# Optimization experiments

Hardware: AMD Instinct MI355X
Metric: run time of the kernel (lower is better)

The kernel has to match this reference:

```python
import jax, jax.numpy as jnp
import numpy as np

EPS = 1e-5


def setup_inputs() -> dict:
    key = jax.random.key(0)
    S, B, I, H, D = 256, 512, 64, 128, 32
    ks = jax.random.split(key, 12)

    def w(k, shape, fan):
        return jax.random.normal(k, shape, jnp.float32) * (fan ** -0.5)

    lengths = jax.random.randint(ks[0], (B,), 1, S + 1)
    lengths = lengths.at[0].set(S)  # ensure max length == S
    return {
        'x': jax.random.normal(ks[1], (S, B, I), jnp.float32),
        'x_d': jax.random.normal(ks[2], (S, B, D), jnp.float32),
        'lengths': lengths,
        'bn_g': jnp.ones((I,), jnp.float32), 'bn_b': jnp.zeros((I,), jnp.float32),
        'bnd_g': jnp.ones((D,), jnp.float32), 'bnd_b': jnp.zeros((D,), jnp.float32),
        'Wih': w(ks[3], (3 * H, I), I), 'Whh': w(ks[4], (3 * H, H), H),
        'bih': jnp.zeros((3 * H,), jnp.float32), 'bhh': jnp.zeros((3 * H,), jnp.float32),
        'attn_W': w(ks[5], (H, H), H), 'attn_b': jnp.zeros((H,), jnp.float32),
        'W1': w(ks[6], (H, H + D), H + D), 'b1': jnp.zeros((H,), jnp.float32),
        'W2': w(ks[7], (H, H), H), 'b2': jnp.zeros((H,), jnp.float32),
        'W3': w(ks[8], (H, H), H), 'b3': jnp.zeros((H,), jnp.float32),
    }


def reference(x, x_d, lengths, bn_g, bn_b, bnd_g, bnd_b, Wih, Whh, bih, bhh,
              attn_W, attn_b, W1, b1, W2, b2, W3, b3):
    S, B, I = x.shape
    H = Whh.shape[1]
    mask = jnp.arange(S)[:, None] < lengths[None, :]          # [S,B] valid-token mask
    mf = mask[..., None].astype(x.dtype)                       # [S,B,1]
    cnt = mf.sum()

    def bn(v, g, b):  # training-mode BatchNorm1d over the packed (valid) tokens
        mu = (v * mf).sum((0, 1)) / cnt
        var = (((v - mu) * mf) ** 2).sum((0, 1)) / cnt
        return (v - mu) * jax.lax.rsqrt(var + EPS) * g + b

    xn = bn(x, bn_g, bn_b)
    xdn = bn(x_d, bnd_g, bnd_b)

    # --- GRU (PyTorch gate order r,z,n) over padded sequence with mask ---
    h0 = jnp.zeros((B, H), x.dtype)

    def step(h, inp):
        xt, mt = inp                                           # xt [B,I], mt [B,1]
        gi = xt @ Wih.T + bih
        gh = h @ Whh.T + bhh
        ir, iz, inn = jnp.split(gi, 3, axis=-1)
        hr, hz, hn = jnp.split(gh, 3, axis=-1)
        r = jax.nn.sigmoid(ir + hr)
        z = jax.nn.sigmoid(iz + hz)
        n = jnp.tanh(inn + r * hn)
        hnew = (1 - z) * n + z * h
        hnext = jnp.where(mt, hnew, h)                         # carry last valid state
        return hnext, jnp.where(mt, hnew, 0.0)                 # padded outputs are 0

    h_last, ys = jax.lax.scan(step, h0, (xn, mf))              # ys [S,B,H]

    # --- Dynamic_Attention: per step i only position j=i survives the causal
    # mask in column k=i, so the dim-0 softmax is over one element -> weight 1.
    # Keep fc in the graph (zero grad, same as torch) via a size-1 softmax. ---
    s = (ys @ attn_W.T + attn_b).sum(-1)                       # [S,B]
    attn = jax.nn.softmax(s[..., None, None], axis=-2)[..., 0, :]  # ones [S,B,1]
    y = attn * ys

    # --- per-token MLP (dropout = identity at eval), vectorized over all tokens ---
    z0 = jnp.concatenate([y, xdn], axis=-1)                    # [S,B,H+D]
    d = jax.nn.relu(z0 @ W1.T + b1)
    d = jax.nn.relu(d @ W2.T + b2)
    d = jax.nn.relu(d @ W3.T + b3)
    out = d * mf                                               # zero padded positions
    return out, h_last[None]                                   # hidden: [1,B,H]
```

## Files before the change

kernel.cpp:

```cpp
#include <hip/hip_runtime.h>
#include <hip/hip_bf16.h>

#define SS 256
#define BB 512
#define II 64
#define HH 128
#define DD 32

typedef __attribute__((ext_vector_type(8))) short short8;
typedef __attribute__((ext_vector_type(4))) float f32x4;

__device__ __forceinline__ short f2bf(float f) {
    unsigned u = __builtin_bit_cast(unsigned, f);
    u += 0x7FFFu + ((u >> 16) & 1u);
    return (short)(u >> 16);
}
__device__ __forceinline__ int pack2bf(float a, float b) {
    return (int)((((unsigned)(unsigned short)f2bf(b)) << 16) |
                  ((unsigned)(unsigned short)f2bf(a)));
}
__device__ __forceinline__ short8 load8bf(const float* p) {
    short8 r;
#pragma unroll
    for (int j = 0; j < 8; ++j) r[j] = f2bf(p[j]);
    return r;
}

__device__ __forceinline__ void sync_lds() {
    __builtin_amdgcn_s_waitcnt(0xc07f);
    __builtin_amdgcn_s_barrier();
}

__global__ __launch_bounds__(256) void stats_kernel(
    const float* __restrict__ x, const float* __restrict__ xd,
    const int* __restrict__ lengths, double* __restrict__ acc,
    unsigned* __restrict__ counter,
    const float* __restrict__ bn_g, const float* __restrict__ bn_b,
    const float* __restrict__ bnd_g, const float* __restrict__ bnd_b,
    float* __restrict__ der)
{
    __shared__ float red_s[256];
    __shared__ float red_q[256];
    __shared__ unsigned s_last;
    const int rows = SS * BB;
    int blk = blockIdx.x;
    const float* v;
    int C, rpb, base;
    if (blk < 256) { v = x;  C = II; rpb = rows / 256; base = 0; }
    else           { v = xd; C = DD; rpb = rows / 128; base = 128; blk -= 256; }

    const int tid = threadIdx.x;
    const int c   = tid & (C - 1);
    const int rg  = tid / C;
    const int rpg = 256 / C;
    const int r0  = blk * rpb;
    const int r1  = r0 + rpb;
    float s = 0.f, q = 0.f;
    for (int r = r0 + rg; r < r1; r += rpg) {
        const int b  = r & (BB - 1);
        const int si = r >> 9;
        if (si < lengths[b]) {
            const float xv = v[(size_t)r * C + c];
            s += xv;
            q  = fmaf(xv, xv, q);
        }
    }
    red_s[tid] = s; red_q[tid] = q;
    __syncthreads();
    if (rg == 0) {
        for (int g = 1; g < rpg; ++g) { s += red_s[c + g * C]; q += red_q[c + g * C]; }
        atomicAdd(&acc[base + c],     (double)s);
        atomicAdd(&acc[base + C + c], (double)q);
    }
    __threadfence();
    __syncthreads();
    if (tid == 0) {
        unsigned old = atomicAdd(counter, 1u);
        s_last = (old == 383u) ? 1u : 0u;
    }
    __syncthreads();
    if (!s_last) return;

    __shared__ int redc[256];
    int cs = 0;
    for (int i = tid; i < BB; i += 256) cs += lengths[i];
    redc[tid] = cs;
    __syncthreads();
    for (int off = 128; off; off >>= 1) {
        if (tid < off) redc[tid] += redc[tid + off];
        __syncthreads();
    }
    const double inv = 1.0 / (double)redc[0];
    if (tid < 64) {
        const double su = __hip_atomic_load(&acc[tid],      __ATOMIC_RELAXED, __HIP_MEMORY_SCOPE_AGENT);
        const double sq = __hip_atomic_load(&acc[64 + tid], __ATOMIC_RELAXED, __HIP_MEMORY_SCOPE_AGENT);
        const double mu  = su * inv;
        const double var = sq * inv - mu * mu;
        const float  rs  = rsqrtf((float)(var + 1e-5));
        const float  a   = rs * bn_g[tid];
        der[tid]      = a;
        der[64 + tid] = bn_b[tid] - (float)mu * a;
    } else if (tid < 96) {
        const int i = tid - 64;
        const double su = __hip_atomic_load(&acc[128 + i], __ATOMIC_RELAXED, __HIP_MEMORY_SCOPE_AGENT);
        const double sq = __hip_atomic_load(&acc[160 + i], __ATOMIC_RELAXED, __HIP_MEMORY_SCOPE_AGENT);
        const double mu  = su * inv;
        const double var = sq * inv - mu * mu;
        const float  rs  = rsqrtf((float)(var + 1e-5));
        const float  a   = rs * bnd_g[i];
        der[128 + i] = a;
        der[160 + i] = bnd_b[i] - (float)mu * a;
    }
}

__global__ __launch_bounds__(512, 2) void gru_kernel(
    const float* __restrict__ x, const int* __restrict__ lengths,
    const float* __restrict__ Wih, const float* __restrict__ Whh,
    const float* __restrict__ bih, const float* __restrict__ bhh,
    const float* __restrict__ der,
    float* __restrict__ ys, float* __restrict__ hlast)
{
    __shared__ __align__(16) short hbf[2][16 * 136];
    __shared__ __align__(16) short xbf[2][16 * 72];

    const int tid  = threadIdx.x;
    const int w    = tid >> 6;
    const int l    = tid & 63;
    const int col  = l & 15;
    const int quad = l >> 4;
    const int b0   = blockIdx.x * 16;
    const int ur   = 16 * w + col;
    const int g0   = 16 * w + quad * 4;

    short8 WR[6], WZ[6], WNh[4], WNx[2];
#pragma unroll
    for (int ks = 0; ks < 4; ++ks) {
        const int ko = ks * 32 + quad * 8;
        WR[ks]  = load8bf(&Whh[(size_t)ur * HH + ko]);
        WZ[ks]  = load8bf(&Whh[(size_t)(HH + ur) * HH + ko]);
        WNh[ks] = load8bf(&Whh[(size_t)(2 * HH + ur) * HH + ko]);
    }
#pragma unroll
    for (int ks = 0; ks < 2; ++ks) {
        const int ko = ks * 32 + quad * 8;
        WR[4 + ks] = load8bf(&Wih[(size_t)ur * II + ko]);
        WZ[4 + ks] = load8bf(&Wih[(size_t)(HH + ur) * II + ko]);
        WNx[ks]    = load8bf(&Wih[(size_t)(2 * HH + ur) * II + ko]);
    }
    float br_[4], bz_[4], bnh_[4], bnx_[4];
#pragma unroll
    for (int r = 0; r < 4; ++r) {
        const int g = g0 + r;
        br_[r]  = bih[g] + bhh[g];
        bz_[r]  = bih[HH + g] + bhh[HH + g];
        bnh_[r] = bhh[2 * HH + g];
        bnx_[r] = bih[2 * HH + g];
    }
    const int len = lengths[b0 + col];

    const int srow = tid >> 5, scol = (tid & 31) * 2;
    const float ax0 = der[scol],      ax1 = der[scol + 1];
    const float cx0 = der[64 + scol], cx1 = der[64 + scol + 1];

    for (int i = tid; i < 16 * 136 / 2; i += 512) ((int*)hbf[0])[i] = 0;
    float hreg[4] = {0.f, 0.f, 0.f, 0.f};
    {
        const float2 xv = *(const float2*)&x[(size_t)(b0 + srow) * II + scol];
        *(int*)&xbf[0][srow * 72 + scol] =
            pack2bf(fmaf(xv.x, ax0, cx0), fmaf(xv.y, ax1, cx1));
    }
    sync_lds();

    int p = 0;
    for (int t = 0; t < SS; ++t) {
        float2 xv;
        if (t + 1 < SS)
            xv = *(const float2*)&x[(size_t)((t + 1) * BB + b0 + srow) * II + scol];

        short8 Hf[4];
#pragma unroll
        for (int ks = 0; ks < 4; ++ks)
            Hf[ks] = *(const short8*)&hbf[p][col * 136 + ks * 32 + quad * 8];
        const short8 XN0 = *(const short8*)&xbf[p][col * 72 + quad * 8];
        const short8 XN1 = *(const short8*)&xbf[p][col * 72 + 32 + quad * 8];

        f32x4 ar  = {br_[0],  br_[1],  br_[2],  br_[3]};
        f32x4 az  = {bz_[0],  bz_[1],  bz_[2],  bz_[3]};
        f32x4 anh = {bnh_[0], bnh_[1], bnh_[2], bnh_[3]};
        f32x4 anx = {bnx_[0], bnx_[1], bnx_[2], bnx_[3]};
#pragma unroll
        for (int ks = 0; ks < 4; ++ks) {
            ar  = __builtin_amdgcn_mfma_f32_16x16x32_bf16(WR[ks],  Hf[ks], ar,  0, 0, 0);
            az  = __builtin_amdgcn_mfma_f32_16x16x32_bf16(WZ[ks],  Hf[ks], az,  0, 0, 0);
            anh = __builtin_amdgcn_mfma_f32_16x16x32_bf16(WNh[ks], Hf[ks], anh, 0, 0, 0);
        }
        ar  = __builtin_amdgcn_mfma_f32_16x16x32_bf16(WR[4],  XN0, ar,  0, 0, 0);
        ar  = __builtin_amdgcn_mfma_f32_16x16x32_bf16(WR[5],  XN1, ar,  0, 0, 0);
        az  = __builtin_amdgcn_mfma_f32_16x16x32_bf16(WZ[4],  XN0, az,  0, 0, 0);
        az  = __builtin_amdgcn_mfma_f32_16x16x32_bf16(WZ[5],  XN1, az,  0, 0, 0);
        anx = __builtin_amdgcn_mfma_f32_16x16x32_bf16(WNx[0], XN0, anx, 0, 0, 0);
        anx = __builtin_amdgcn_mfma_f32_16x16x32_bf16(WNx[1], XN1, anx, 0, 0, 0);

        const bool valid = (t < len);
#pragma unroll
        for (int r = 0; r < 4; ++r) {
            const float rg = __builtin_amdgcn_rcpf(1.f + __expf(-ar[r]));
            const float zg = __builtin_amdgcn_rcpf(1.f + __expf(-az[r]));
            const float nv = anx[r] + rg * anh[r];
            const float ng = 1.f - 2.f * __builtin_amdgcn_rcpf(1.f + __expf(2.f * nv));
            const float hnew = (1.f - zg) * ng + zg * hreg[r];
            hreg[r] = valid ? hnew : hreg[r];
        }
        {
            float4 o;
            o.x = hreg[0]; o.y = hreg[1]; o.z = hreg[2]; o.w = hreg[3];
            *(float4*)&ys[((size_t)t * BB + b0 + col) * HH + g0] = o;
            int2 pk;
            pk.x = pack2bf(hreg[0], hreg[1]);
            pk.y = pack2bf(hreg[2], hreg[3]);
            *(int2*)&hbf[p ^ 1][col * 136 + g0] = pk;
        }
        if (t + 1 < SS)
            *(int*)&xbf[p ^ 1][srow * 72 + scol] =
                pack2bf(fmaf(xv.x, ax0, cx0), fmaf(xv.y, ax1, cx1));

        sync_lds();
        p ^= 1;
    }

    {
        float4 hl;
        hl.x = hreg[0]; hl.y = hreg[1]; hl.z = hreg[2]; hl.w = hreg[3];
        *(float4*)&hlast[(size_t)(b0 + col) * HH + g0] = hl;
    }
}

__global__ __launch_bounds__(512, 2) void mlp_kernel(
    const float* __restrict__ xd, const int* __restrict__ lengths,
    const float* __restrict__ W1, const float* __restrict__ b1v,
    const float* __restrict__ W2, const float* __restrict__ b2v,
    const float* __restrict__ W3, const float* __restrict__ b3v,
    const float* __restrict__ der, float* io)
{
    __shared__ __align__(16) short z0[2][16 * 168];
    __shared__ __align__(16) short d1b[2][16 * 136];
    __shared__ __align__(16) short d2b[2][16 * 136];

    const int tid  = threadIdx.x;
    const int w    = tid >> 6;
    const int l    = tid & 63;
    const int col  = l & 15;
    const int quad = l >> 4;
    const int ur   = 16 * w + col;
    const int g0   = 16 * w + quad * 4;

    short8 F1[5], F2[4], F3[4];
#pragma unroll
    for (int ks = 0; ks < 5; ++ks)
        F1[ks] = load8bf(&W1[(size_t)ur * 160 + ks * 32 + quad * 8]);
#pragma unroll
    for (int ks = 0; ks < 4; ++ks) {
        const int ko = ks * 32 + quad * 8;
        F2[ks] = load8bf(&W2[(size_t)ur * HH + ko]);
        F3[ks] = load8bf(&W3[(size_t)ur * HH + ko]);
    }
    float bb1_[4], bb2_[4], bb3_[4];
#pragma unroll
    for (int r = 0; r < 4; ++r) {
        bb1_[r] = b1v[g0 + r]; bb2_[r] = b2v[g0 + r]; bb3_[r] = b3v[g0 + r];
    }

    const int yrow = tid >> 5, yc = (tid & 31) * 4;
    const int drow = tid >> 4, dcol = (tid & 15) * 2;
    float ad0 = 0.f, ad1 = 0.f, cd0 = 0.f, cd1 = 0.f;
    if (tid < 256) {
        ad0 = der[128 + dcol]; ad1 = der[128 + dcol + 1];
        cd0 = der[160 + dcol]; cd1 = der[160 + dcol + 1];
    }

    const int tile0 = blockIdx.x * 16;

    {
        const size_t tok0 = (size_t)tile0 * 16;
        const float4 yv = *(const float4*)&io[(tok0 + yrow) * HH + yc];
        int2 pk;
        pk.x = pack2bf(yv.x, yv.y);
        pk.y = pack2bf(yv.z, yv.w);
        *(int2*)&z0[0][yrow * 168 + yc] = pk;
        if (tid < 256) {
            const float2 dv = *(const float2*)&xd[(tok0 + drow) * DD + dcol];
            *(int*)&z0[0][drow * 168 + HH + dcol] =
                pack2bf(fmaf(dv.x, ad0, cd0), fmaf(dv.y, ad1, cd1));
        }
    }
    sync_lds();

    int p = 0;
    for (int it = 0; it <= 17; ++it) {
        float4 yv; float2 dv;
        const int nt = it + 1;
        if (nt <= 15) {
            const size_t tok0n = (size_t)(tile0 + nt) * 16;
            yv = *(const float4*)&io[(tok0n + yrow) * HH + yc];
            if (tid < 256) dv = *(const float2*)&xd[(tok0n + drow) * DD + dcol];
        }

        f32x4 a1 = {bb1_[0], bb1_[1], bb1_[2], bb1_[3]};
#pragma unroll
        for (int ks = 0; ks < 5; ++ks)
            a1 = __builtin_amdgcn_mfma_f32_16x16x32_bf16(
                F1[ks], *(const short8*)&z0[p][col * 168 + ks * 32 + quad * 8], a1, 0, 0, 0);
        {
            int2 pk;
            pk.x = pack2bf(fmaxf(a1[0], 0.f), fmaxf(a1[1], 0.f));
            pk.y = pack2bf(fmaxf(a1[2], 0.f), fmaxf(a1[3], 0.f));
            *(int2*)&d1b[p ^ 1][col * 136 + g0] = pk;
        }

        f32x4 a2 = {bb2_[0], bb2_[1], bb2_[2], bb2_[3]};
#pragma unroll
        for (int ks = 0; ks < 4; ++ks)
            a2 = __builtin_amdgcn_mfma_f32_16x16x32_bf16(
                F2[ks], *(const short8*)&d1b[p][col * 136 + ks * 32 + quad * 8], a2, 0, 0, 0);
        {
            int2 pk;
            pk.x = pack2bf(fmaxf(a2[0], 0.f), fmaxf(a2[1], 0.f));
            pk.y = pack2bf(fmaxf(a2[2], 0.f), fmaxf(a2[3], 0.f));
            *(int2*)&d2b[p ^ 1][col * 136 + g0] = pk;
        }

        f32x4 a3 = {bb3_[0], bb3_[1], bb3_[2], bb3_[3]};
#pragma unroll
        for (int ks = 0; ks < 4; ++ks)
            a3 = __builtin_amdgcn_mfma_f32_16x16x32_bf16(
                F3[ks], *(const short8*)&d2b[p][col * 136 + ks * 32 + quad * 8], a3, 0, 0, 0);
        if (it >= 2) {
            const int tok0 = (tile0 + it - 2) * 16;
            const int tI = tok0 >> 9;
            const int bI = tok0 & (BB - 1);
            const bool v = tI < lengths[bI + col];
            float4 o;
            o.x = v ? fmaxf(a3[0], 0.f) : 0.f;
            o.y = v ? fmaxf(a3[1], 0.f) : 0.f;
            o.z = v ? fmaxf(a3[2], 0.f) : 0.f;
            o.w = v ? fmaxf(a3[3], 0.f) : 0.f;
            *(float4*)&io[((size_t)tok0 + col) * HH + g0] = o;
        }

        if (nt <= 15) {
            int2 pk;
            pk.x = pack2bf(yv.x, yv.y);
            pk.y = pack2bf(yv.z, yv.w);
            *(int2*)&z0[p ^ 1][yrow * 168 + yc] = pk;
            if (tid < 256)
                *(int*)&z0[p ^ 1][drow * 168 + HH + dcol] =
                    pack2bf(fmaf(dv.x, ad0, cd0), fmaf(dv.y, ad1, cd1));
        }
        sync_lds();
        p ^= 1;
    }
}

extern "C" void kernel_launch(void* const* d_in, const int* in_sizes, int n_in,
                              void* d_out, int out_size, void* d_ws, size_t ws_size,
                              hipStream_t stream)
{
    (void)in_sizes; (void)n_in; (void)out_size; (void)ws_size;
    const float* x     = (const float*)d_in[0];
    const float* xd    = (const float*)d_in[1];
    const int*   lens  = (const int*)d_in[2];
    const float* bn_g  = (const float*)d_in[3];
    const float* bn_b  = (const float*)d_in[4];
    const float* bnd_g = (const float*)d_in[5];
    const float* bnd_b = (const float*)d_in[6];
    const float* Wih   = (const float*)d_in[7];
    const float* Whh   = (const float*)d_in[8];
    const float* bih   = (const float*)d_in[9];
    const float* bhh   = (const float*)d_in[10];
    const float* W1    = (const float*)d_in[13];
    const float* b1    = (const float*)d_in[14];
    const float* W2    = (const float*)d_in[15];
    const float* b2    = (const float*)d_in[16];
    const float* W3    = (const float*)d_in[17];
    const float* b3    = (const float*)d_in[18];

    float* out   = (float*)d_out;
    float* hlast = out + (size_t)SS * BB * HH;

    double*   acc     = (double*)d_ws;
    unsigned* counter = (unsigned*)((char*)d_ws + 1536);
    float*    der     = (float*)((char*)d_ws + 2048);

    (void)hipMemsetAsync(d_ws, 0, 2048, stream);

    stats_kernel<<<384, 256, 0, stream>>>(x, xd, lens, acc, counter,
                                          bn_g, bn_b, bnd_g, bnd_b, der);

    gru_kernel<<<BB / 16, 512, 0, stream>>>(x, lens, Wih, Whh, bih, bhh, der,
                                            out, hlast);

    mlp_kernel<<<512, 512, 0, stream>>>(xd, lens, W1, b1, W2, b2, W3, b3,
                                        der, out);
}
```

Measured before the change: 478.9 us.

## Fuse per-token MLP into GRU recurrence with a three-stage software pipeline

The separate MLP kernel is merged into the GRU kernel. Each timestep's hidden state, still in LDS as bf16, feeds the three MLP layers, staggered over the following steps. This avoids writing the fp32 GRU outputs to global memory and reading them back, and drops one kernel launch. In exchange, every recurrent step carries extra MFMAs and LDS traffic. The MLP weights also stay resident in registers alongside the GRU weights, which risks register spills under the 512x2 launch bound and a longer serial critical path.

```diff
diff --git a/kernel.cpp b/kernel.cpp
--- a/kernel.cpp
+++ b/kernel.cpp
@@ -113,15 +113,22 @@
     }
 }
 
-__global__ __launch_bounds__(512, 2) void gru_kernel(
-    const float* __restrict__ x, const int* __restrict__ lengths,
+__global__ __launch_bounds__(512, 2) void gru_mlp_kernel(
+    const float* __restrict__ x, const float* __restrict__ xd,
+    const int* __restrict__ lengths,
     const float* __restrict__ Wih, const float* __restrict__ Whh,
     const float* __restrict__ bih, const float* __restrict__ bhh,
+    const float* __restrict__ W1, const float* __restrict__ b1v,
+    const float* __restrict__ W2, const float* __restrict__ b2v,
+    const float* __restrict__ W3, const float* __restrict__ b3v,
     const float* __restrict__ der,
-    float* __restrict__ ys, float* __restrict__ hlast)
+    float* __restrict__ out, float* __restrict__ hlast)
 {
     __shared__ __align__(16) short hbf[2][16 * 136];
     __shared__ __align__(16) short xbf[2][16 * 72];
+    __shared__ __align__(16) short xdb[2][16 * 40];
+    __shared__ __align__(16) short d1b[2][16 * 136];
+    __shared__ __align__(16) short d2b[2][16 * 136];
 
     const int tid  = threadIdx.x;
     const int w    = tid >> 6;
@@ -147,7 +154,17 @@
         WZ[4 + ks] = load8bf(&Wih[(size_t)(HH + ur) * II + ko]);
         WNx[ks]    = load8bf(&Wih[(size_t)(2 * HH + ur) * II + ko]);
     }
-    float br_[4], bz_[4], bnh_[4], bnx_[4];
+    short8 F1[5], F2[4], F3[4];
+#pragma unroll
+    for (int ks = 0; ks < 5; ++ks)
+        F1[ks] = load8bf(&W1[(size_t)ur * 160 + ks * 32 + quad * 8]);
+#pragma unroll
+    for (int ks = 0; ks < 4; ++ks) {
+        const int ko = ks * 32 + quad * 8;
+        F2[ks] = load8bf(&W2[(size_t)ur * HH + ko]);
+        F3[ks] = load8bf(&W3[(size_t)ur * HH + ko]);
+    }
+    float br_[4], bz_[4], bnh_[4], bnx_[4], bb1_[4], bb2_[4], bb3_[4];
 #pragma unroll
     for (int r = 0; r < 4; ++r) {
         const int g = g0 + r;
@@ -155,12 +172,19 @@
         bz_[r]  = bih[HH + g] + bhh[HH + g];
         bnh_[r] = bhh[2 * HH + g];
         bnx_[r] = bih[2 * HH + g];
+        bb1_[r] = b1v[g]; bb2_[r] = b2v[g]; bb3_[r] = b3v[g];
     }
     const int len = lengths[b0 + col];
 
     const int srow = tid >> 5, scol = (tid & 31) * 2;
     const float ax0 = der[scol],      ax1 = der[scol + 1];
     const float cx0 = der[64 + scol], cx1 = der[64 + scol + 1];
+    const int drow = tid >> 4, dcol = (tid & 15) * 2;
+    float ad0 = 0.f, ad1 = 0.f, cd0 = 0.f, cd1 = 0.f;
+    if (tid < 256) {
+        ad0 = der[128 + dcol]; ad1 = der[128 + dcol + 1];
+        cd0 = der[160 + dcol]; cd1 = der[160 + dcol + 1];
+    }
 
     for (int i = tid; i < 16 * 136 / 2; i += 512) ((int*)hbf[0])[i] = 0;
     float hreg[4] = {0.f, 0.f, 0.f, 0.f};
@@ -172,192 +196,112 @@
     sync_lds();
 
     int p = 0;
-    for (int t = 0; t < SS; ++t) {
-        float2 xv;
+    for (int t = 0; t < SS + 3; ++t) {
+        float2 xv, dv;
         if (t + 1 < SS)
             xv = *(const float2*)&x[(size_t)((t + 1) * BB + b0 + srow) * II + scol];
+        if (t < SS && tid < 256)
+            dv = *(const float2*)&xd[(size_t)((size_t)t * BB + b0 + drow) * DD + dcol];
 
         short8 Hf[4];
-#pragma unroll
-        for (int ks = 0; ks < 4; ++ks)
-            Hf[ks] = *(const short8*)&hbf[p][col * 136 + ks * 32 + quad * 8];
-        const short8 XN0 = *(const short8*)&xbf[p][col * 72 + quad * 8];
-        const short8 XN1 = *(const short8*)&xbf[p][col * 72 + 32 + quad * 8];
-
-        f32x4 ar  = {br_[0],  br_[1],  br_[2],  br_[3]};
-        f32x4 az  = {bz_[0],  bz_[1],  bz_[2],  bz_[3]};
-        f32x4 anh = {bnh_[0], bnh_[1], bnh_[2], bnh_[3]};
-        f32x4 anx = {bnx_[0], bnx_[1], bnx_[2], bnx_[3]};
-#pragma unroll
-        for (int ks = 0; ks < 4; ++ks) {
-            ar  = __builtin_amdgcn_mfma_f32_16x16x32_bf16(WR[ks],  Hf[ks], ar,  0, 0, 0);
-            az  = __builtin_amdgcn_mfma_f32_16x16x32_bf16(WZ[ks],  Hf[ks], az,  0, 0, 0);
-            anh = __builtin_amdgcn_mfma_f32_16x16x32_bf16(WNh[ks], Hf[ks], anh, 0, 0, 0);
-        }
-        ar  = __builtin_amdgcn_mfma_f32_16x16x32_bf16(WR[4],  XN0, ar,  0, 0, 0);
-        ar  = __builtin_amdgcn_mfma_f32_16x16x32_bf16(WR[5],  XN1, ar,  0, 0, 0);
-        az  = __builtin_amdgcn_mfma_f32_16x16x32_bf16(WZ[4],  XN0, az,  0, 0, 0);
-        az  = __builtin_amdgcn_mfma_f32_16x16x32_bf16(WZ[5],  XN1, az,  0, 0, 0);
-        anx = __builtin_amdgcn_mfma_f32_16x16x32_bf16(WNx[0], XN0, anx, 0, 0, 0);
-        anx = __builtin_amdgcn_mfma_f32_16x16x32_bf16(WNx[1], XN1, anx, 0, 0, 0);
-
-        const bool valid = (t < len);
-#pragma unroll
-        for (int r = 0; r < 4; ++r) {
-            const float rg = __builtin_amdgcn_rcpf(1.f + __expf(-ar[r]));
-            const float zg = __builtin_amdgcn_rcpf(1.f + __expf(-az[r]));
-            const float nv = anx[r] + rg * anh[r];
-            const float ng = 1.f - 2.f * __builtin_amdgcn_rcpf(1.f + __expf(2.f * nv));
-            const float hnew = (1.f - zg) * ng + zg * hreg[r];
-            hreg[r] = valid ? hnew : hreg[r];
-        }
-        {
-            float4 o;
-            o.x = hreg[0]; o.y = hreg[1]; o.z = hreg[2]; o.w = hreg[3];
-            *(float4*)&ys[((size_t)t * BB + b0 + col) * HH + g0] = o;
+        if (t <= SS) {
+#pragma unroll
+            for (int ks = 0; ks < 4; ++ks)
+                Hf[ks] = *(const short8*)&hbf[p][col * 136 + ks * 32 + quad * 8];
+        }
+
+        if (t < SS) {
+            const short8 XN0 = *(const short8*)&xbf[p][col * 72 + quad * 8];
+            const short8 XN1 = *(const short8*)&xbf[p][col * 72 + 32 + quad * 8];
+
+            f32x4 ar  = {br_[0],  br_[1],  br_[2],  br_[3]};
+            f32x4 az  = {bz_[0],  bz_[1],  bz_[2],  bz_[3]};
+            f32x4 anh = {bnh_[0], bnh_[1], bnh_[2], bnh_[3]};
+            f32x4 anx = {bnx_[0], bnx_[1], bnx_[2], bnx_[3]};
+#pragma unroll
+            for (int ks = 0; ks < 4; ++ks) {
+                ar  = __builtin_amdgcn_mfma_f32_16x16x32_bf16(WR[ks],  Hf[ks], ar,  0, 0, 0);
+                az  = __builtin_amdgcn_mfma_f32_16x16x32_bf16(WZ[ks],  Hf[ks], az,  0, 0, 0);
+                anh = __builtin_amdgcn_mfma_f32_16x16x32_bf16(WNh[ks], Hf[ks], anh, 0, 0, 0);
+            }
+            ar  = __builtin_amdgcn_mfma_f32_16x16x32_bf16(WR[4],  XN0, ar,  0, 0, 0);
+            ar  = __builtin_amdgcn_mfma_f32_16x16x32_bf16(WR[5],  XN1, ar,  0, 0, 0);
+            az  = __builtin_amdgcn_mfma_f32_16x16x32_bf16(WZ[4],  XN0, az,  0, 0, 0);
+            az  = __builtin_amdgcn_mfma_f32_16x16x32_bf16(WZ[5],  XN1, az,  0, 0, 0);
+            anx = __builtin_amdgcn_mfma_f32_16x16x32_bf16(WNx[0], XN0, anx, 0, 0, 0);
+            anx = __builtin_amdgcn_mfma_f32_16x16x32_bf16(WNx[1], XN1, anx, 0, 0, 0);
+
+            const bool valid = (t < len);
+#pragma unroll
+            for (int r = 0; r < 4; ++r) {
+                const float rg = __builtin_amdgcn_rcpf(1.f + __expf(-ar[r]));
+                const float zg = __builtin_amdgcn_rcpf(1.f + __expf(-az[r]));
+                const float nv = anx[r] + rg * anh[r];
+                const float ng = 1.f - 2.f * __builtin_amdgcn_rcpf(1.f + __expf(2.f * nv));
+                const float hnew = (1.f - zg) * ng + zg * hreg[r];
+                hreg[r] = valid ? hnew : hreg[r];
+            }
             int2 pk;
             pk.x = pack2bf(hreg[0], hreg[1]);
             pk.y = pack2bf(hreg[2], hreg[3]);
             *(int2*)&hbf[p ^ 1][col * 136 + g0] = pk;
         }
-        if (t + 1 < SS)
-            *(int*)&xbf[p ^ 1][srow * 72 + scol] =
-                pack2bf(fmaf(xv.x, ax0, cx0), fmaf(xv.y, ax1, cx1));
-
-        sync_lds();
-        p ^= 1;
-    }
-
-    {
-        float4 hl;
-        hl.x = hreg[0]; hl.y = hreg[1]; hl.z = hreg[2]; hl.w = hreg[3];
-        *(float4*)&hlast[(size_t)(b0 + col) * HH + g0] = hl;
-    }
-}
-
-__global__ __launch_bounds__(512, 2) void mlp_kernel(
-    const float* __restrict__ xd, const int* __restrict__ lengths,
-    const float* __restrict__ W1, const float* __restrict__ b1v,
-    const float* __restrict__ W2, const float* __restrict__ b2v,
-    const float* __restrict__ W3, const float* __restrict__ b3v,
-    const float* __restrict__ der, float* io)
-{
-    __shared__ __align__(16) short z0[2][16 * 168];
-    __shared__ __align__(16) short d1b[2][16 * 136];
-    __shared__ __align__(16) short d2b[2][16 * 136];
-
-    const int tid  = threadIdx.x;
-    const int w    = tid >> 6;
-    const int l    = tid & 63;
-    const int col  = l & 15;
-    const int quad = l >> 4;
-    const int ur   = 16 * w + col;
-    const int g0   = 16 * w + quad * 4;
-
-    short8 F1[5], F2[4], F3[4];
-#pragma unroll
-    for (int ks = 0; ks < 5; ++ks)
-        F1[ks] = load8bf(&W1[(size_t)ur * 160 + ks * 32 + quad * 8]);
-#pragma unroll
-    for (int ks = 0; ks < 4; ++ks) {
-        const int ko = ks * 32 + quad * 8;
-        F2[ks] = load8bf(&W2[(size_t)ur * HH + ko]);
-        F3[ks] = load8bf(&W3[(size_t)ur * HH + ko]);
-    }
-    float bb1_[4], bb2_[4], bb3_[4];
-#pragma unroll
-    for (int r = 0; r < 4; ++r) {
-        bb1_[r] = b1v[g0 + r]; bb2_[r] = b2v[g0 + r]; bb3_[r] = b3v[g0 + r];
-    }
-
-    const int yrow = tid >> 5, yc = (tid & 31) * 4;
-    const int drow = tid >> 4, dcol = (tid & 15) * 2;
-    float ad0 = 0.f, ad1 = 0.f, cd0 = 0.f, cd1 = 0.f;
-    if (tid < 256) {
-        ad0 = der[128 + dcol]; ad1 = der[128 + dcol + 1];
-        cd0 = der[160 + dcol]; cd1 = der[160 + dcol + 1];
-    }
-
-    const int tile0 = blockIdx.x * 16;
-
-    {
-        const size_t tok0 = (size_t)tile0 * 16;
-        const float4 yv = *(const float4*)&io[(tok0 + yrow) * HH + yc];
-        int2 pk;
-        pk.x = pack2bf(yv.x, yv.y);
-        pk.y = pack2bf(yv.z, yv.w);
-        *(int2*)&z0[0][yrow * 168 + yc] = pk;
-        if (tid < 256) {
-            const float2 dv = *(const float2*)&xd[(tok0 + drow) * DD + dcol];
-            *(int*)&z0[0][drow * 168 + HH + dcol] =
-                pack2bf(fmaf(dv.x, ad0, cd0), fmaf(dv.y, ad1, cd1));
-        }
-    }
-    sync_lds();
-
-    int p = 0;
-    for (int it = 0; it <= 17; ++it) {
-        float4 yv; float2 dv;
-        const int nt = it + 1;
-        if (nt <= 15) {
-            const size_t tok0n = (size_t)(tile0 + nt) * 16;
-            yv = *(const float4*)&io[(tok0n + yrow) * HH + yc];
-            if (tid < 256) dv = *(const float2*)&xd[(tok0n + drow) * DD + dcol];
-        }
-
-        f32x4 a1 = {bb1_[0], bb1_[1], bb1_[2], bb1_[3]};
-#pragma unroll
-        for (int ks = 0; ks < 5; ++ks)
-            a1 = __builtin_amdgcn_mfma_f32_16x16x32_bf16(
-                F1[ks], *(const short8*)&z0[p][col * 168 + ks * 32 + quad * 8], a1, 0, 0, 0);
-        {
+
+        if (t >= 1 && t <= SS) {
+            const short8 XD = *(const short8*)&xdb[p][col * 40 + quad * 8];
+            f32x4 a1 = {bb1_[0], bb1_[1], bb1_[2], bb1_[3]};
+#pragma unroll
+            for (int ks = 0; ks < 4; ++ks)
+                a1 = __builtin_amdgcn_mfma_f32_16x16x32_bf16(F1[ks], Hf[ks], a1, 0, 0, 0);
+            a1 = __builtin_amdgcn_mfma_f32_16x16x32_bf16(F1[4], XD, a1, 0, 0, 0);
             int2 pk;
             pk.x = pack2bf(fmaxf(a1[0], 0.f), fmaxf(a1[1], 0.f));
             pk.y = pack2bf(fmaxf(a1[2], 0.f), fmaxf(a1[3], 0.f));
             *(int2*)&d1b[p ^ 1][col * 136 + g0] = pk;
         }
 
-        f32x4 a2 = {bb2_[0], bb2_[1], bb2_[2], bb2_[3]};
-#pragma unroll
-        for (int ks = 0; ks < 4; ++ks)
-            a2 = __builtin_amdgcn_mfma_f32_16x16x32_bf16(
-                F2[ks], *(const short8*)&d1b[p][col * 136 + ks * 32 + quad * 8], a2, 0, 0, 0);
-        {
+        if (t >= 2 && t <= SS + 1) {
+            f32x4 a2 = {bb2_[0], bb2_[1], bb2_[2], bb2_[3]};
+#pragma unroll
+            for (int ks = 0; ks < 4; ++ks)
+                a2 = __builtin_amdgcn_mfma_f32_16x16x32_bf16(
+                    F2[ks], *(const short8*)&d1b[p][col * 136 + ks * 32 + quad * 8], a2, 0, 0, 0);
             int2 pk;
             pk.x = pack2bf(fmaxf(a2[0], 0.f), fmaxf(a2[1], 0.f));
             pk.y = pack2bf(fmaxf(a2[2], 0.f), fmaxf(a2[3], 0.f));
             *(int2*)&d2b[p ^ 1][col * 136 + g0] = pk;
         }
 
-        f32x4 a3 = {bb3_[0], bb3_[1], bb3_[2], bb3_[3]};
-#pragma unroll
-        for (int ks = 0; ks < 4; ++ks)
-            a3 = __builtin_amdgcn_mfma_f32_16x16x32_bf16(
-                F3[ks], *(const short8*)&d2b[p][col * 136 + ks * 32 + quad * 8], a3, 0, 0, 0);
-        if (it >= 2) {
-            const int tok0 = (tile0 + it - 2) * 16;
-            const int tI = tok0 >> 9;
-            const int bI = tok0 & (BB - 1);
-            const bool v = tI < lengths[bI + col];
+        if (t >= 3) {
+            f32x4 a3 = {bb3_[0], bb3_[1], bb3_[2], bb3_[3]};
+#pragma unroll
+            for (int ks = 0; ks < 4; ++ks)
+                a3 = __builtin_amdgcn_mfma_f32_16x16x32_bf16(
+                    F3[ks], *(const short8*)&d2b[p][col * 136 + ks * 32 + quad * 8], a3, 0, 0, 0);
+            const bool v = (t - 3) < len;
             float4 o;
             o.x = v ? fmaxf(a3[0], 0.f) : 0.f;
             o.y = v ? fmaxf(a3[1], 0.f) : 0.f;
             o.z = v ? fmaxf(a3[2], 0.f) : 0.f;
             o.w = v ? fmaxf(a3[3], 0.f) : 0.f;
-            *(float4*)&io[((size_t)tok0 + col) * HH + g0] = o;
-        }
-
-        if (nt <= 15) {
-            int2 pk;
-            pk.x = pack2bf(yv.x, yv.y);
-            pk.y = pack2bf(yv.z, yv.w);
-            *(int2*)&z0[p ^ 1][yrow * 168 + yc] = pk;
-            if (tid < 256)
-                *(int*)&z0[p ^ 1][drow * 168 + HH + dcol] =
-                    pack2bf(fmaf(dv.x, ad0, cd0), fmaf(dv.y, ad1, cd1));
-        }
+            *(float4*)&out[((size_t)(t - 3) * BB + b0 + col) * HH + g0] = o;
+        }
+
+        if (t + 1 < SS)
+            *(int*)&xbf[p ^ 1][srow * 72 + scol] =
+                pack2bf(fmaf(xv.x, ax0, cx0), fmaf(xv.y, ax1, cx1));
+        if (t < SS && tid < 256)
+            *(int*)&xdb[p ^ 1][drow * 40 + dcol] =
+                pack2bf(fmaf(dv.x, ad0, cd0), fmaf(dv.y, ad1, cd1));
+
         sync_lds();
         p ^= 1;
+    }
+
+    {
+        float4 hl;
+        hl.x = hreg[0]; hl.y = hreg[1]; hl.z = hreg[2]; hl.w = hreg[3];
+        *(float4*)&hlast[(size_t)(b0 + col) * HH + g0] = hl;
     }
 }
 
@@ -396,9 +340,7 @@
     stats_kernel<<<384, 256, 0, stream>>>(x, xd, lens, acc, counter,
                                           bn_g, bn_b, bnd_g, bnd_b, der);
 
-    gru_kernel<<<BB / 16, 512, 0, stream>>>(x, lens, Wih, Whh, bih, bhh, der,
-                                            out, hlast);
-
-    mlp_kernel<<<512, 512, 0, stream>>>(xd, lens, W1, b1, W2, b2, W3, b3,
-                                        der, out);
-}
+    gru_mlp_kernel<<<BB / 16, 512, 0, stream>>>(x, xd, lens, Wih, Whh, bih, bhh,
+                                                W1, b1, W2, b2, W3, b3,
+                                                der, out, hlast);
+}
```

New measurement: 674.1 us. 40.8% more time.
